# Optimization experiments

Hardware: AMD Instinct MI355X
Metric: run time of the kernel (lower is better)

## Reference

```python
import jax, jax.numpy as jnp
import numpy as np

D_MODEL = 1024
NUM_HEADS = 16
D_K = D_MODEL // NUM_HEADS
BLOCK_SIZE = 64
SPARSITY_FACTOR = 4


def sparse_mask(seq_len):
    i = jnp.arange(seq_len)[:, None]
    j = jnp.arange(seq_len)[None, :]
    local = jnp.abs(j - i) <= BLOCK_SIZE // 2  # window [i-32, i+32]
    strided = (j % SPARSITY_FACTOR) == (i % SPARSITY_FACTOR)
    return local | strided  # [S, S] bool


def setup_inputs() -> dict:
    key = jax.random.key(0)
    ks = jax.random.split(key, 9)
    s = 1.0 / np.sqrt(D_MODEL)
    x = jax.random.normal(ks[0], (2, 2048, D_MODEL), dtype=jnp.float32)
    Wq = jax.random.normal(ks[1], (D_MODEL, D_MODEL), dtype=jnp.float32) * s
    Wk = jax.random.normal(ks[2], (D_MODEL, D_MODEL), dtype=jnp.float32) * s
    Wv = jax.random.normal(ks[3], (D_MODEL, D_MODEL), dtype=jnp.float32) * s
    Wo = jax.random.normal(ks[4], (D_MODEL, D_MODEL), dtype=jnp.float32) * s
    bq = jax.random.normal(ks[5], (D_MODEL,), dtype=jnp.float32) * 0.01
    bk = jax.random.normal(ks[6], (D_MODEL,), dtype=jnp.float32) * 0.01
    bv = jax.random.normal(ks[7], (D_MODEL,), dtype=jnp.float32) * 0.01
    bo = jax.random.normal(ks[8], (D_MODEL,), dtype=jnp.float32) * 0.01
    return {"x": x, "Wq": Wq, "bq": bq, "Wk": Wk, "bk": bk,
            "Wv": Wv, "bv": bv, "Wo": Wo, "bo": bo}


def reference(x, Wq, bq, Wk, bk, Wv, bv, Wo, bo):
    B, S, _ = x.shape
    # nn.Linear: y = x @ W.T + b
    def heads(W, b):
        return (x @ W.T + b).reshape(B, S, NUM_HEADS, D_K).transpose(0, 2, 1, 3)
    Q = heads(Wq, bq)  # [B,H,S,Dk]
    K = heads(Wk, bk)
    V = heads(Wv, bv)
    scores = jnp.einsum('bhsd,bhtd->bhst', Q, K) / np.sqrt(D_K)  # [B,H,S,S]
    mask = sparse_mask(S)  # [S,S]
    scores = jnp.where(mask[None, None], scores, -jnp.inf)
    probs = jax.nn.softmax(scores, axis=-1)
    out = jnp.einsum('bhst,bhtd->bhsd', probs, V)  # [B,H,S,Dk]
    out = out.transpose(0, 2, 1, 3).reshape(B, S, D_MODEL)
    return out @ Wo.T + bo
```

## Files before the change

### kernel.cpp

```cpp
#include <hip/hip_runtime.h>

typedef unsigned short ushort_t;
typedef __bf16 bf16x8 __attribute__((ext_vector_type(8)));
typedef float  f32x4  __attribute__((ext_vector_type(4)));

#define MFMA16(a,b,c) __builtin_amdgcn_mfma_f32_16x16x32_bf16((a),(b),(c),0,0,0)

__device__ __forceinline__ ushort_t f2bf(float f) {
    union { float f; unsigned u; } x; x.f = f;
    unsigned r = (x.u + 0x7fffu + ((x.u >> 16) & 1u)) >> 16;
    return (ushort_t)r;
}

__device__ __forceinline__ void gload16(const ushort_t* g, char* l) {
    __builtin_amdgcn_global_load_lds(
        (const __attribute__((address_space(1))) unsigned*)g,
        (__attribute__((address_space(3))) unsigned*)l, 16, 0, 0);
}

__global__ void cast_all(const float* __restrict__ x,
                         const float* __restrict__ Wq, const float* __restrict__ Wk,
                         const float* __restrict__ Wv, const float* __restrict__ Wo,
                         ushort_t* __restrict__ xbf, ushort_t* __restrict__ wqkv,
                         ushort_t* __restrict__ wob) {
    int i = blockIdx.x * 256 + threadIdx.x;
    float4 v;
    if (i < 1048576) {
        v = ((const float4*)x)[i];
        ushort4 o;
        o.x = f2bf(v.x); o.y = f2bf(v.y); o.z = f2bf(v.z); o.w = f2bf(v.w);
        ((ushort4*)xbf)[i] = o;
    } else {
        int j = i - 1048576;
        int r = j >> 18, jj = j & 0x3ffff;
        const float* src = (r == 0) ? Wq : (r == 1) ? Wk : (r == 2) ? Wv : Wo;
        v = ((const float4*)src)[jj];
        ushort4 o;
        o.x = f2bf(v.x); o.y = f2bf(v.y); o.z = f2bf(v.z); o.w = f2bf(v.w);
        if (r < 3) ((ushort4*)wqkv)[(size_t)r*262144 + jj] = o;
        else       ((ushort4*)wob)[jj] = o;
    }
}

__global__ void gemm_qkv(const ushort_t* __restrict__ A,
                         const ushort_t* __restrict__ Bw,
                         const float* __restrict__ b0, const float* __restrict__ b1,
                         const float* __restrict__ b2,
                         void* __restrict__ C0, void* __restrict__ C1,
                         void* __restrict__ C2)
{
    __shared__ __align__(16) char lds[32768];
    char* As = lds;
    char* Bs = lds + 16384;
    const int tid  = threadIdx.x;
    const int lane = tid & 63;
    const int wid  = tid >> 6;
    const int wrow = wid >> 1;
    const int wcol = wid & 1;
    const int l15  = lane & 15;
    const int lhi  = lane >> 4;
    const int m0 = blockIdx.x * 128;
    const int n0 = blockIdx.y * 128;

    f32x4 acc[4][4] = {};

    #define STAGE(kb)                                                          \
        _Pragma("unroll")                                                      \
        for (int k = 0; k < 4; ++k) {                                          \
            int idx = k*256 + tid;                                             \
            int row = idx >> 3, s = idx & 7;                                   \
            int sc = s ^ (row & 7);                                            \
            gload16(A  + (size_t)(m0+row)*1024 + (kb) + sc*8, As + idx*16);    \
            gload16(Bw + (size_t)(n0+row)*1024 + (kb) + sc*8, Bs + idx*16);    \
        }

    STAGE(0)
    for (int kt = 0; kt < 16; ++kt) {
        __syncthreads();
        #pragma unroll
        for (int ks = 0; ks < 2; ++ks) {
            bf16x8 af[4], bfr[4];
            #pragma unroll
            for (int i = 0; i < 4; ++i) {
                int row = wrow*64 + i*16 + l15;
                int sl  = ks*4 + lhi;
                af[i] = *(const bf16x8*)(As + row*128 + ((sl ^ (row & 7)) << 4));
            }
            #pragma unroll
            for (int j = 0; j < 4; ++j) {
                int row = wcol*64 + j*16 + l15;
                int sl  = ks*4 + lhi;
                bfr[j] = *(const bf16x8*)(Bs + row*128 + ((sl ^ (row & 7)) << 4));
            }
            #pragma unroll
            for (int i = 0; i < 4; ++i)
                #pragma unroll
                for (int j = 0; j < 4; ++j)
                    acc[i][j] = MFMA16(af[i], bfr[j], acc[i][j]);
        }
        __syncthreads();
        if (kt < 15) STAGE((kt+1)*64)
    }
    #undef STAGE

    const int reg  = n0 >> 10;
    const int nnw0 = (n0 & 1023) + wcol*64;
    const int h    = nnw0 >> 6;
    const int b    = (m0 + wrow*64) >> 11;
    const int s0w  = (m0 + wrow*64) & 2047;
    const size_t hh = (size_t)b*16 + h;
    const float* bp = (reg == 0) ? b0 : (reg == 1) ? b1 : b2;
    const float qsc = (reg == 0) ? 0.125f : 1.0f;
    char* Cw = lds + wid*8192;

    if (reg == 2) {
        #pragma unroll
        for (int i = 0; i < 4; ++i)
            #pragma unroll
            for (int j = 0; j < 4; ++j)
                #pragma unroll
                for (int q = 0; q < 4; ++q) {
                    float v = acc[i][j][q] + bp[nnw0 + j*16 + l15];
                    int rowl = j*16 + l15;
                    int cb = (q*16 + i*4 + lhi) * 2;
                    *(__bf16*)(Cw + rowl*128 + (cb & 15) + ((((cb >> 4)) ^ (rowl & 7)) << 4)) = (__bf16)v;
                }
    } else {
        #pragma unroll
        for (int i = 0; i < 4; ++i)
            #pragma unroll
            for (int j = 0; j < 4; ++j)
                #pragma unroll
                for (int q = 0; q < 4; ++q) {
                    float v = (acc[i][j][q] + bp[nnw0 + j*16 + l15]) * qsc;
                    int rowl = i*16 + lhi*4 + q;
                    int cb = (j*16 + l15) * 2;
                    *(__bf16*)(Cw + rowl*128 + (cb & 15) + ((((cb >> 4)) ^ (rowl & 7)) << 4)) = (__bf16)v;
                }
    }
    __syncthreads();

    const int rowr = lane >> 3;
    const int sl2  = lane & 7;
    #pragma unroll
    for (int p = 0; p < 8; ++p) {
        int row = p*8 + rowr;
        bf16x8 val = *(const bf16x8*)(Cw + row*128 + ((sl2 ^ (row & 7)) << 4));
        ushort_t* dst;
        if (reg == 0) {
            dst = (ushort_t*)C0 + (hh*2048 + s0w + row)*64 + sl2*8;
        } else if (reg == 1) {
            dst = (ushort_t*)C1 + ((hh*4 + (row & 3))*512 + (s0w >> 2) + (row >> 2))*64 + sl2*8;
        } else {
            dst = (ushort_t*)C2 + ((hh*4 + (sl2 >> 1))*64 + row)*512 + (s0w >> 2) + (sl2 & 1)*8;
        }
        *(bf16x8*)dst = val;
    }
}

__global__ void gemm_o(const ushort_t* __restrict__ A,
                       const ushort_t* __restrict__ Bw,
                       const float* __restrict__ b0,
                       float* __restrict__ C0)
{
    __shared__ __align__(16) char lds[24576];
    char* As = lds;
    char* Bs = lds + 8192;
    const int tid  = threadIdx.x;
    const int lane = tid & 63;
    const int wid  = tid >> 6;
    const int wrow = wid >> 1;
    const int wcol = wid & 1;
    const int l15  = lane & 15;
    const int lhi  = lane >> 4;
    const int m0 = blockIdx.x * 64;
    const int n0 = blockIdx.y * 128;

    f32x4 acc[2][4] = {};

    #define STAGEO(kb)                                                         \
        _Pragma("unroll")                                                      \
        for (int k = 0; k < 2; ++k) {                                          \
            int idx = k*256 + tid;                                             \
            int row = idx >> 3, s = idx & 7;                                   \
            int sc = s ^ (row & 7);                                            \
            gload16(A + (size_t)(m0+row)*1024 + (kb) + sc*8, As + idx*16);     \
        }                                                                      \
        _Pragma("unroll")                                                      \
        for (int k = 0; k < 4; ++k) {                                          \
            int idx = k*256 + tid;                                             \
            int row = idx >> 3, s = idx & 7;                                   \
            int sc = s ^ (row & 7);                                            \
            gload16(Bw + (size_t)(n0+row)*1024 + (kb) + sc*8, Bs + idx*16);    \
        }

    STAGEO(0)
    for (int kt = 0; kt < 16; ++kt) {
        __syncthreads();
        #pragma unroll
        for (int ks = 0; ks < 2; ++ks) {
            bf16x8 af[2], bfr[4];
            #pragma unroll
            for (int i = 0; i < 2; ++i) {
                int row = wrow*32 + i*16 + l15;
                int sl  = ks*4 + lhi;
                af[i] = *(const bf16x8*)(As + row*128 + ((sl ^ (row & 7)) << 4));
            }
            #pragma unroll
            for (int j = 0; j < 4; ++j) {
                int row = wcol*64 + j*16 + l15;
                int sl  = ks*4 + lhi;
                bfr[j] = *(const bf16x8*)(Bs + row*128 + ((sl ^ (row & 7)) << 4));
            }
            #pragma unroll
            for (int i = 0; i < 2; ++i)
                #pragma unroll
                for (int j = 0; j < 4; ++j)
                    acc[i][j] = MFMA16(af[i], bfr[j], acc[i][j]);
        }
        __syncthreads();
        if (kt < 15) STAGEO((kt+1)*64)
    }
    #undef STAGEO

    #pragma unroll
    for (int i = 0; i < 2; ++i)
        #pragma unroll
        for (int j = 0; j < 4; ++j)
            #pragma unroll
            for (int q = 0; q < 4; ++q) {
                int gm = m0 + wrow*32 + i*16 + lhi*4 + q;
                int gn = n0 + wcol*64 + j*16 + l15;
                C0[(size_t)gm*1024 + gn] = acc[i][j][q] + b0[gn];
            }
}

__global__ __launch_bounds__(256, 2)
void sparse_attn8(const ushort_t* __restrict__ Qg,
                  const ushort_t* __restrict__ Kss,
                  const ushort_t* __restrict__ Vts,
                  ushort_t* __restrict__ attn)
{
    __shared__ __align__(16) char Klds[2][8192];
    __shared__ __align__(16) char Vlds[2][8192];
    __shared__ __align__(16) char Ps[8192];
    const int tid  = threadIdx.x;
    const int lane = tid & 63;
    const int w    = tid >> 6;
    const int l15  = lane & 15;
    const int lhi  = lane >> 4;
    const int id2  = (blockIdx.x & 7)*128 + (blockIdx.x >> 3);
    const int bh   = id2 >> 5;
    const int rem  = id2 & 31;
    const int r    = rem >> 3;
    const int g    = rem & 7;
    char* Pw = Ps + w*2048;

    const ushort_t* Kst0 = Kss + (size_t)bh*4*512*64;
    const ushort_t* Vts0 = Vts + (size_t)bh*4*64*512;
    const ushort_t* Kst  = Kst0 + (size_t)r*512*64;
    const ushort_t* Vst  = Vts0 + (size_t)r*64*512;

    const int bl0 = (g > 0) ? 4*g - 1 : 0;
    const int bl1 = (g < 7) ? 4*g + 4 : 31;
    const int NT  = 8 + (bl1 - bl0 + 1);

    bf16x8 aq[2];
    {
        const ushort_t* qp = Qg + ((size_t)bh*2048 + r + 4*(g*64 + w*16 + l15))*64 + lhi*8;
        aq[0] = *(const bf16x8*)(qp);
        aq[1] = *(const bf16x8*)(qp + 32);
    }

    float tsum[4] = {0.f, 0.f, 0.f, 0.f};
    f32x4 oacc[4] = {};

    #define ASTAGE(t, b)                                                           \
        _Pragma("unroll")                                                          \
        for (int k = 0; k < 2; ++k) {                                              \
            int idx = k*256 + tid;                                                 \
            int row = idx >> 3, s = idx & 7;                                       \
            int sc = s ^ (row & 7);                                                \
            if ((t) < 8) {                                                         \
                gload16(Kst + (size_t)((t)*64 + row)*64 + sc*8, &Klds[b][idx*16]); \
                gload16(Vst + (size_t)row*512 + (t)*64 + sc*8, &Vlds[b][idx*16]);  \
            } else {                                                               \
                int bl = bl0 + (t) - 8;                                            \
                gload16(Kst0 + (size_t)((row>>4)*512 + bl*16 + (row&15))*64 + sc*8,\
                        &Klds[b][idx*16]);                                         \
                gload16(Vts0 + (size_t)((sc>>1)*64 + row)*512 + bl*16 + (sc&1)*8,  \
                        &Vlds[b][idx*16]);                                         \
            }                                                                      \
        }

    ASTAGE(0, 0)
    int cur = 0;
    for (int t = 0; t < NT; ++t) {
        __syncthreads();
        if (t + 1 < NT) ASTAGE(t + 1, cur ^ 1)
        f32x4 sacc[4] = {};
        #pragma unroll
        for (int ks = 0; ks < 2; ++ks) {
            bf16x8 bk[4];
            #pragma unroll
            for (int n = 0; n < 4; ++n) {
                int row = n*16 + l15;
                int sl  = ks*4 + lhi;
                bk[n] = *(const bf16x8*)(&Klds[cur][row*128 + ((sl ^ (row & 7)) << 4)]);
            }
            #pragma unroll
            for (int n = 0; n < 4; ++n)
                sacc[n] = MFMA16(aq[ks], bk[n], sacc[n]);
        }
        if (t < 8) {
            #pragma unroll
            for (int n = 0; n < 4; ++n) {
                int colb = (n*16 + l15) * 2;
                #pragma unroll
                for (int q = 0; q < 4; ++q) {
                    float p = __expf(sacc[n][q] - 16.f);
                    tsum[q] += p;
                    int rowp = lhi*4 + q;
                    *(__bf16*)(Pw + rowp*128 + (colb ^ ((rowp & 7) << 4))) = (__bf16)p;
                }
            }
        } else {
            int bl = bl0 + t - 8;
            #pragma unroll
            for (int n = 0; n < 4; ++n) {
                int j = 4*(bl*16 + l15) + n;
                int colb = (n*16 + l15) * 2;
                bool nres = (n != r);
                #pragma unroll
                for (int q = 0; q < 4; ++q) {
                    int i = r + 4*(g*64 + w*16 + 4*lhi + q);
                    int d = j - i;
                    bool valid = nres && (d <= 32) && (d >= -32);
                    float sv = valid ? sacc[n][q] : -1e30f;
                    float p = __expf(sv - 16.f);
                    tsum[q] += p;
                    int rowp = lhi*4 + q;
                    *(__bf16*)(Pw + rowp*128 + (colb ^ ((rowp & 7) << 4))) = (__bf16)p;
                }
            }
        }
        #pragma unroll
        for (int ks = 0; ks < 2; ++ks) {
            int sl = ks*4 + lhi;
            bf16x8 pf = *(const bf16x8*)(Pw + l15*128 + ((sl ^ (l15 & 7)) << 4));
            #pragma unroll
            for (int d = 0; d < 4; ++d) {
                int rowv = d*16 + l15;
                bf16x8 vf = *(const bf16x8*)(&Vlds[cur][rowv*128 + ((sl ^ (rowv & 7)) << 4)]);
                oacc[d] = MFMA16(pf, vf, oacc[d]);
            }
        }
        cur ^= 1;
    }
    #undef ASTAGE

    const int b = bh >> 4, h = bh & 15;
    f32x4 invv;
    #pragma unroll
    for (int q = 0; q < 4; ++q) {
        float t = tsum[q];
        t += __shfl_xor(t, 1);
        t += __shfl_xor(t, 2);
        t += __shfl_xor(t, 4);
        t += __shfl_xor(t, 8);
        invv[q] = 1.f / t;
    }
    #pragma unroll
    for (int d = 0; d < 4; ++d) {
        f32x4 o = oacc[d] * invv;
        #pragma unroll
        for (int q = 0; q < 4; ++q) {
            int srow = r + 4*(g*64 + w*16 + 4*lhi + q);
            int gr = b*2048 + srow;
            int gc = h*64 + d*16 + l15;
            attn[(size_t)gr*1024 + gc] = f2bf(o[q]);
        }
    }
}

extern "C" void kernel_launch(void* const* d_in, const int* in_sizes, int n_in,
                              void* d_out, int out_size, void* d_ws, size_t ws_size,
                              hipStream_t stream)
{
    const float* x  = (const float*)d_in[0];
    const float* Wq = (const float*)d_in[1];
    const float* bq = (const float*)d_in[2];
    const float* Wk = (const float*)d_in[3];
    const float* bk = (const float*)d_in[4];
    const float* Wv = (const float*)d_in[5];
    const float* bv = (const float*)d_in[6];
    const float* Wo = (const float*)d_in[7];
    const float* bo = (const float*)d_in[8];

    char* ws = (char*)d_ws;
    ushort_t* xbf  = (ushort_t*)(ws);
    ushort_t* wqkv = (ushort_t*)(ws + ((size_t)8  << 20));
    ushort_t* wob  = (ushort_t*)(ws + ((size_t)14 << 20));
    ushort_t* Qb   = (ushort_t*)(ws + ((size_t)16 << 20));
    ushort_t* Kss  = (ushort_t*)(ws + ((size_t)24 << 20));
    ushort_t* Vts  = (ushort_t*)(ws + ((size_t)32 << 20));
    ushort_t* attn = (ushort_t*)(ws + ((size_t)40 << 20));

    cast_all<<<8192, 256, 0, stream>>>(x, Wq, Wk, Wv, Wo, xbf, wqkv, wob);

    gemm_qkv<<<dim3(32, 24), 256, 0, stream>>>(xbf, wqkv, bq, bk, bv,
                                               Qb, Kss, Vts);

    sparse_attn8<<<dim3(1024), 256, 0, stream>>>(Qb, Kss, Vts, attn);

    gemm_o<<<dim3(64, 8), 256, 0, stream>>>(attn, wob, bo, (float*)d_out);
}
```

Baseline: 91.44 us.

## Double-buffer GEMM LDS tiles with BK=32 and add MFMA priority hints in attention

Measured after the change: 95.89 us. 1.05x slower.

```diff
diff --git a/kernel.cpp b/kernel.cpp
--- a/kernel.cpp
+++ b/kernel.cpp
@@ -17,6 +17,9 @@
         (const __attribute__((address_space(1))) unsigned*)g,
         (__attribute__((address_space(3))) unsigned*)l, 16, 0, 0);
 }
+
+#define SW_RD(row, s)  (((s) + (((row) >> 1) & 3)) & 3)
+#define SW_SRC(row, s) (((s) + 4 - (((row) >> 1) & 3)) & 3)
 
 __global__ void cast_all(const float* __restrict__ x,
                          const float* __restrict__ Wq, const float* __restrict__ Wk,
@@ -50,8 +53,10 @@
                          void* __restrict__ C2)
 {
     __shared__ __align__(16) char lds[32768];
-    char* As = lds;
-    char* Bs = lds + 16384;
+    char* const As0 = lds;
+    char* const Bs0 = lds + 8192;
+    char* const As1 = lds + 16384;
+    char* const Bs1 = lds + 24576;
     const int tid  = threadIdx.x;
     const int lane = tid & 63;
     const int wid  = tid >> 6;
@@ -64,44 +69,48 @@
 
     f32x4 acc[4][4] = {};
 
-    #define STAGE(kb)                                                          \
+    #define STG(dA, dB, kb)                                                    \
         _Pragma("unroll")                                                      \
-        for (int k = 0; k < 4; ++k) {                                          \
+        for (int k = 0; k < 2; ++k) {                                          \
             int idx = k*256 + tid;                                             \
-            int row = idx >> 3, s = idx & 7;                                   \
-            int sc = s ^ (row & 7);                                            \
-            gload16(A  + (size_t)(m0+row)*1024 + (kb) + sc*8, As + idx*16);    \
-            gload16(Bw + (size_t)(n0+row)*1024 + (kb) + sc*8, Bs + idx*16);    \
-        }
-
-    STAGE(0)
-    for (int kt = 0; kt < 16; ++kt) {
+            int row = idx >> 2, s = idx & 3;                                   \
+            int sc = SW_SRC(row, s);                                           \
+            gload16(A  + (size_t)(m0+row)*1024 + (kb) + sc*8, (dA) + idx*16);  \
+            gload16(Bw + (size_t)(n0+row)*1024 + (kb) + sc*8, (dB) + idx*16);  \
+        }
+
+    #define CMP(sA, sB)                                                        \
+        {                                                                      \
+            bf16x8 af[4], bfr[4];                                              \
+            _Pragma("unroll")                                                  \
+            for (int i = 0; i < 4; ++i) {                                      \
+                int row = wrow*64 + i*16 + l15;                                \
+                af[i] = *(const bf16x8*)((sA) + row*64 + (SW_RD(row, lhi) << 4)); \
+            }                                                                  \
+            _Pragma("unroll")                                                  \
+            for (int j = 0; j < 4; ++j) {                                      \
+                int row = wcol*64 + j*16 + l15;                                \
+                bfr[j] = *(const bf16x8*)((sB) + row*64 + (SW_RD(row, lhi) << 4)); \
+            }                                                                  \
+            _Pragma("unroll")                                                  \
+            for (int i = 0; i < 4; ++i)                                        \
+                _Pragma("unroll")                                              \
+                for (int j = 0; j < 4; ++j)                                    \
+                    acc[i][j] = MFMA16(af[i], bfr[j], acc[i][j]);              \
+        }
+
+    STG(As0, Bs0, 0)
+    __syncthreads();
+    for (int kp = 0; kp < 16; ++kp) {
+        STG(As1, Bs1, (2*kp+1)*32)
+        CMP(As0, Bs0)
         __syncthreads();
-        #pragma unroll
-        for (int ks = 0; ks < 2; ++ks) {
-            bf16x8 af[4], bfr[4];
-            #pragma unroll
-            for (int i = 0; i < 4; ++i) {
-                int row = wrow*64 + i*16 + l15;
-                int sl  = ks*4 + lhi;
-                af[i] = *(const bf16x8*)(As + row*128 + ((sl ^ (row & 7)) << 4));
-            }
-            #pragma unroll
-            for (int j = 0; j < 4; ++j) {
-                int row = wcol*64 + j*16 + l15;
-                int sl  = ks*4 + lhi;
-                bfr[j] = *(const bf16x8*)(Bs + row*128 + ((sl ^ (row & 7)) << 4));
-            }
-            #pragma unroll
-            for (int i = 0; i < 4; ++i)
-                #pragma unroll
-                for (int j = 0; j < 4; ++j)
-                    acc[i][j] = MFMA16(af[i], bfr[j], acc[i][j]);
-        }
+        if (kp < 15) STG(As0, Bs0, (2*kp+2)*32)
+        CMP(As1, Bs1)
         __syncthreads();
-        if (kt < 15) STAGE((kt+1)*64)
-    }
-    #undef STAGE
+    }
+    #undef STG
+    #undef CMP
 
     const int reg  = n0 >> 10;
     const int nnw0 = (n0 & 1023) + wcol*64;
@@ -164,8 +173,10 @@
                        float* __restrict__ C0)
 {
     __shared__ __align__(16) char lds[24576];
-    char* As = lds;
-    char* Bs = lds + 8192;
+    char* const As0 = lds;
+    char* const Bs0 = lds + 4096;
+    char* const As1 = lds + 12288;
+    char* const Bs1 = lds + 16384;
     const int tid  = threadIdx.x;
     const int lane = tid & 63;
     const int wid  = tid >> 6;
@@ -178,50 +189,52 @@
 
     f32x4 acc[2][4] = {};
 
-    #define STAGEO(kb)                                                         \
-        _Pragma("unroll")                                                      \
-        for (int k = 0; k < 2; ++k) {                                          \
-            int idx = k*256 + tid;                                             \
-            int row = idx >> 3, s = idx & 7;                                   \
-            int sc = s ^ (row & 7);                                            \
-            gload16(A + (size_t)(m0+row)*1024 + (kb) + sc*8, As + idx*16);     \
-        }                                                                      \
-        _Pragma("unroll")                                                      \
-        for (int k = 0; k < 4; ++k) {                                          \
-            int idx = k*256 + tid;                                             \
-            int row = idx >> 3, s = idx & 7;                                   \
-            int sc = s ^ (row & 7);                                            \
-            gload16(Bw + (size_t)(n0+row)*1024 + (kb) + sc*8, Bs + idx*16);    \
-        }
-
-    STAGEO(0)
-    for (int kt = 0; kt < 16; ++kt) {
+    #define STGO(dA, dB, kb)                                                   \
+        {                                                                      \
+            int rowA = tid >> 2, sA_ = tid & 3;                                \
+            int scA = SW_SRC(rowA, sA_);                                       \
+            gload16(A + (size_t)(m0+rowA)*1024 + (kb) + scA*8, (dA) + tid*16); \
+            _Pragma("unroll")                                                  \
+            for (int k = 0; k < 2; ++k) {                                      \
+                int idx = k*256 + tid;                                         \
+                int row = idx >> 2, s = idx & 3;                               \
+                int sc = SW_SRC(row, s);                                       \
+                gload16(Bw + (size_t)(n0+row)*1024 + (kb) + sc*8, (dB) + idx*16); \
+            }                                                                  \
+        }
+
+    #define CMPO(sA, sB)                                                       \
+        {                                                                      \
+            bf16x8 af[2], bfr[4];                                              \
+            _Pragma("unroll")                                                  \
+            for (int i = 0; i < 2; ++i) {                                      \
+                int row = wrow*32 + i*16 + l15;                                \
+                af[i] = *(const bf16x8*)((sA) + row*64 + (SW_RD(row, lhi) << 4)); \
+            }                                                                  \
+            _Pragma("unroll")                                                  \
+            for (int j = 0; j < 4; ++j) {                                      \
+                int row = wcol*64 + j*16 + l15;                                \
+                bfr[j] = *(const bf16x8*)((sB) + row*64 + (SW_RD(row, lhi) << 4)); \
+            }                                                                  \
+            _Pragma("unroll")                                                  \
+            for (int i = 0; i < 2; ++i)                                        \
+                _Pragma("unroll")                                              \
+                for (int j = 0; j < 4; ++j)                                    \
+                    acc[i][j] = MFMA16(af[i], bfr[j], acc[i][j]);              \
+        }
+
+    STGO(As0, Bs0, 0)
+    __syncthreads();
+    for (int kp = 0; kp < 16; ++kp) {
+        STGO(As1, Bs1, (2*kp+1)*32)
+        CMPO(As0, Bs0)
         __syncthreads();
-        #pragma unroll
-        for (int ks = 0; ks < 2; ++ks) {
-            bf16x8 af[2], bfr[4];
-            #pragma unroll
-            for (int i = 0; i < 2; ++i) {
-                int row = wrow*32 + i*16 + l15;
-                int sl  = ks*4 + lhi;
-                af[i] = *(const bf16x8*)(As + row*128 + ((sl ^ (row & 7)) << 4));
-            }
-            #pragma unroll
-            for (int j = 0; j < 4; ++j) {
-                int row = wcol*64 + j*16 + l15;
-                int sl  = ks*4 + lhi;
-                bfr[j] = *(const bf16x8*)(Bs + row*128 + ((sl ^ (row & 7)) << 4));
-            }
-            #pragma unroll
-            for (int i = 0; i < 2; ++i)
-                #pragma unroll
-                for (int j = 0; j < 4; ++j)
-                    acc[i][j] = MFMA16(af[i], bfr[j], acc[i][j]);
-        }
+        if (kp < 15) STGO(As0, Bs0, (2*kp+2)*32)
+        CMPO(As1, Bs1)
         __syncthreads();
-        if (kt < 15) STAGEO((kt+1)*64)
-    }
-    #undef STAGEO
+    }
+    #undef STGO
+    #undef CMPO
 
     #pragma unroll
     for (int i = 0; i < 2; ++i)
@@ -299,6 +312,7 @@
         __syncthreads();
         if (t + 1 < NT) ASTAGE(t + 1, cur ^ 1)
         f32x4 sacc[4] = {};
+        __builtin_amdgcn_s_setprio(1);
         #pragma unroll
         for (int ks = 0; ks < 2; ++ks) {
             bf16x8 bk[4];
@@ -312,6 +326,7 @@
             for (int n = 0; n < 4; ++n)
                 sacc[n] = MFMA16(aq[ks], bk[n], sacc[n]);
         }
+        __builtin_amdgcn_s_setprio(0);
         if (t < 8) {
             #pragma unroll
             for (int n = 0; n < 4; ++n) {
@@ -344,6 +359,7 @@
                 }
             }
         }
+        __builtin_amdgcn_s_setprio(1);
         #pragma unroll
         for (int ks = 0; ks < 2; ++ks) {
             int sl = ks*4 + lhi;
@@ -355,6 +371,7 @@
                 oacc[d] = MFMA16(pf, vf, oacc[d]);
             }
         }
+        __builtin_amdgcn_s_setprio(0);
         cur ^= 1;
     }
     #undef ASTAGE
```
